# Optimization experiments

Hardware: AMD Instinct MI355X
Metric: run time of the kernel (lower is better)

Reference implementation:

```python
import jax, jax.numpy as jnp
import numpy as np

N, C, Wd, Hd = 16, 64, 128, 128


def setup_inputs() -> dict:
    key = jax.random.key(0)
    k = jax.random.split(key, 6)
    return {
        "xR": jax.random.normal(k[0], (N, C, Wd, Hd), dtype=jnp.float32),
        "xT": jax.random.normal(k[1], (N, C, Wd, Hd), dtype=jnp.float32),
        "WR": jax.random.normal(k[2], (C, C), dtype=jnp.float32) * 0.05,
        "bR": jax.random.normal(k[3], (C,), dtype=jnp.float32) * 0.05,
        "WT": jax.random.normal(k[4], (C, C), dtype=jnp.float32) * 0.05,
        "bT": jax.random.normal(k[5], (C,), dtype=jnp.float32) * 0.05,
    }


def reference(xR, xT, WR, bR, WT, bT):
    n, c, w, h = xR.shape
    wh = w * h
    # 1x1 convs (weight [out_c, in_c]) + bias
    xRa = jnp.einsum('nchw,dc->ndhw', xR, WR) + bR[None, :, None, None]
    xTa = jnp.einsum('nchw,dc->ndhw', xT, WT) + bT[None, :, None, None]
    # [N, WH, C] views of adjusted features
    r = xRa.transpose(0, 2, 3, 1).reshape(n, wh, c)
    t = xTa.transpose(0, 2, 3, 1).reshape(n, wh, c)
    # channel self-attention: [N, C, C] = r^T @ r (reduce over WH)
    rs = jnp.einsum('npc,npd->ncd', r, r)
    ts = jnp.einsum('npc,npd->ncd', t, t)
    # concat along channel-row axis and softmax over the 2C rows
    att = jax.nn.softmax(jnp.concatenate([rs, ts], axis=1), axis=1)  # [N, 2C, C]
    # original (unadjusted) features concatenated along channels: [N, WH, 2C]
    rO = xR.transpose(0, 2, 3, 1).reshape(n, wh, c)
    tO = xT.transpose(0, 2, 3, 1).reshape(n, wh, c)
    xO = jnp.concatenate([rO, tO], axis=2)
    out = jnp.einsum('npk,nkc->npc', xO, att)  # [N, WH, C]
    return out.reshape(n, w, h, c).transpose(0, 3, 1, 2)
```

## Files before the change

### kernel.cpp

```cpp
#include <hip/hip_runtime.h>
#include <math.h>

#define WH 16384

typedef __attribute__((ext_vector_type(8))) short short8;
typedef __attribute__((ext_vector_type(4))) float f32x4;

__device__ __forceinline__ void atomAddF(float* p, float v) {
    __hip_atomic_fetch_add(p, v, __ATOMIC_RELAXED, __HIP_MEMORY_SCOPE_AGENT);
}
__device__ __forceinline__ unsigned short f2bf(float x) {
    unsigned u = __float_as_uint(x);
    u += 0x7fff + ((u >> 16) & 1);
    return (unsigned short)(u >> 16);
}
__device__ __forceinline__ float bf2f(unsigned short h) {
    return __uint_as_float(((unsigned)h) << 16);
}

__global__ void zero_ws_kernel(float* __restrict__ p, int n) {
    int i = blockIdx.x * 256 + threadIdx.x;
    if (i < n) p[i] = 0.f;
}

__global__ __launch_bounds__(256, 2) void gram_kernel(
    const float* __restrict__ xR, const float* __restrict__ xT,
    float* __restrict__ G, float* __restrict__ sv) {
    __shared__ unsigned short shi[16384];
    __shared__ unsigned short slo[16384];
    const int t = threadIdx.x, w = t >> 6, lane = t & 63;
    const int n = blockIdx.y, inp = blockIdx.z;
    const float* __restrict__ X = (inp ? xT : xR) + (size_t)n * 64 * WH;
    float* __restrict__ Gout = G + (size_t)(inp * 16 + n) * 4096;
    float* __restrict__ Sout = sv + (size_t)(inp * 16 + n) * 64;
    const int pbase = blockIdx.x << 10;

    f32x4 acc0 = {0.f, 0.f, 0.f, 0.f}, acc1 = acc0, acc2 = acc0, acc3 = acc0;
    float srow[16];
#pragma unroll
    for (int i = 0; i < 16; ++i) srow[i] = 0.f;

    const int g2 = lane >> 1, halfo = (lane & 1) << 2;
    const int m15 = lane & 15, q = lane >> 4;
    const int cha = (w << 4) + m15;
    const int ch0 = m15, ch1 = 16 + m15, ch2 = 32 + m15, ch3 = 48 + m15;

    float4 vbuf[16];
#pragma unroll
    for (int i = 0; i < 16; ++i) {
        const int r = (i << 2) + w;
        vbuf[i] = *(const float4*)(X + (size_t)r * WH + pbase + (lane << 2));
    }

    for (int tile = 0; tile < 4; ++tile) {
        __syncthreads();
#pragma unroll
        for (int i = 0; i < 16; ++i) {
            const int r = (i << 2) + w;
            const float4 v = vbuf[i];
            srow[i] += v.x + v.y + v.z + v.w;
            const unsigned short h0 = f2bf(v.x), h1 = f2bf(v.y), h2 = f2bf(v.z), h3 = f2bf(v.w);
            const unsigned short l0 = f2bf(v.x - bf2f(h0)), l1 = f2bf(v.y - bf2f(h1)),
                                 l2 = f2bf(v.z - bf2f(h2)), l3 = f2bf(v.w - bf2f(h3));
            const int a = (r << 8) + ((g2 ^ (r & 31)) << 3) + halfo;
            *(ushort4*)&shi[a] = make_ushort4(h0, h1, h2, h3);
            *(ushort4*)&slo[a] = make_ushort4(l0, l1, l2, l3);
        }
        __syncthreads();
        if (tile < 3) {
            const int p1 = pbase + ((tile + 1) << 8);
#pragma unroll
            for (int i = 0; i < 16; ++i) {
                const int r = (i << 2) + w;
                vbuf[i] = *(const float4*)(X + (size_t)r * WH + p1 + (lane << 2));
            }
        }
#pragma unroll
        for (int kk = 0; kk < 8; ++kk) {
            const int grp = (kk << 2) + q;
            const int offa = (cha << 8) + ((grp ^ (cha & 31)) << 3);
            const int off0 = (ch0 << 8) + ((grp ^ (ch0 & 31)) << 3);
            const int off1 = (ch1 << 8) + ((grp ^ (ch1 & 31)) << 3);
            const int off2 = (ch2 << 8) + ((grp ^ (ch2 & 31)) << 3);
            const int off3 = (ch3 << 8) + ((grp ^ (ch3 & 31)) << 3);
            const short8 ah = *(const short8*)&shi[offa];
            const short8 al = *(const short8*)&slo[offa];
            const short8 bh0 = *(const short8*)&shi[off0], bl0 = *(const short8*)&slo[off0];
            const short8 bh1 = *(const short8*)&shi[off1], bl1 = *(const short8*)&slo[off1];
            const short8 bh2 = *(const short8*)&shi[off2], bl2 = *(const short8*)&slo[off2];
            const short8 bh3 = *(const short8*)&shi[off3], bl3 = *(const short8*)&slo[off3];
            acc0 = __builtin_amdgcn_mfma_f32_16x16x32_bf16(ah, bh0, acc0, 0, 0, 0);
            acc0 = __builtin_amdgcn_mfma_f32_16x16x32_bf16(ah, bl0, acc0, 0, 0, 0);
            acc0 = __builtin_amdgcn_mfma_f32_16x16x32_bf16(al, bh0, acc0, 0, 0, 0);
            acc0 = __builtin_amdgcn_mfma_f32_16x16x32_bf16(al, bl0, acc0, 0, 0, 0);
            acc1 = __builtin_amdgcn_mfma_f32_16x16x32_bf16(ah, bh1, acc1, 0, 0, 0);
            acc1 = __builtin_amdgcn_mfma_f32_16x16x32_bf16(ah, bl1, acc1, 0, 0, 0);
            acc1 = __builtin_amdgcn_mfma_f32_16x16x32_bf16(al, bh1, acc1, 0, 0, 0);
            acc1 = __builtin_amdgcn_mfma_f32_16x16x32_bf16(al, bl1, acc1, 0, 0, 0);
            acc2 = __builtin_amdgcn_mfma_f32_16x16x32_bf16(ah, bh2, acc2, 0, 0, 0);
            acc2 = __builtin_amdgcn_mfma_f32_16x16x32_bf16(ah, bl2, acc2, 0, 0, 0);
            acc2 = __builtin_amdgcn_mfma_f32_16x16x32_bf16(al, bh2, acc2, 0, 0, 0);
            acc2 = __builtin_amdgcn_mfma_f32_16x16x32_bf16(al, bl2, acc2, 0, 0, 0);
            acc3 = __builtin_amdgcn_mfma_f32_16x16x32_bf16(ah, bh3, acc3, 0, 0, 0);
            acc3 = __builtin_amdgcn_mfma_f32_16x16x32_bf16(ah, bl3, acc3, 0, 0, 0);
            acc3 = __builtin_amdgcn_mfma_f32_16x16x32_bf16(al, bh3, acc3, 0, 0, 0);
            acc3 = __builtin_amdgcn_mfma_f32_16x16x32_bf16(al, bl3, acc3, 0, 0, 0);
        }
    }
    const int rb = (w << 4) + (q << 2);
#pragma unroll
    for (int r = 0; r < 4; ++r) {
        atomAddF(&Gout[(rb + r) * 64 + 0 + m15], acc0[r]);
        atomAddF(&Gout[(rb + r) * 64 + 16 + m15], acc1[r]);
        atomAddF(&Gout[(rb + r) * 64 + 32 + m15], acc2[r]);
        atomAddF(&Gout[(rb + r) * 64 + 48 + m15], acc3[r]);
    }
#pragma unroll
    for (int i = 0; i < 16; ++i) {
        float v = srow[i];
        for (int m = 32; m >= 1; m >>= 1) v += __shfl_xor(v, m, 64);
        if (lane == 0) atomAddF(&Sout[(i << 2) + w], v);
    }
}

__global__ __launch_bounds__(256) void logits_softmax_kernel(
    const float* __restrict__ WR, const float* __restrict__ bR,
    const float* __restrict__ WT, const float* __restrict__ bT,
    const float* __restrict__ G, const float* __restrict__ sv,
    unsigned short* __restrict__ attb) {
    __shared__ float ldsW[4096];
    __shared__ float ldsWt[4096];
    __shared__ float ldsG[4096];
    __shared__ float ldsL[8192];
    __shared__ float ldsS[64], ldsU[64], ldsMx[64], ldsInv[64];
    const int t = threadIdx.x, n = blockIdx.x;
    for (int inp = 0; inp < 2; ++inp) {
        const float* __restrict__ W = inp ? WT : WR;
        const float* __restrict__ b = inp ? bT : bR;
        const float* __restrict__ Gn = G + (size_t)(inp * 16 + n) * 4096;
        const float* __restrict__ sn = sv + (size_t)(inp * 16 + n) * 64;
        __syncthreads();
#pragma unroll
        for (int m = 0; m < 16; ++m) {
            const int idx = t + (m << 8);
            const float wv = W[idx];
            ldsW[idx] = wv;
            ldsWt[((idx & 63) << 6) + (idx >> 6)] = wv;
            ldsG[idx] = Gn[idx];
        }
        if (t < 64) ldsS[t] = sn[t];
        __syncthreads();
        if (t < 64) {
            float u = 0.f;
            for (int c = 0; c < 64; ++c) u += ldsW[(t << 6) + c] * ldsS[c];
            ldsU[t] = u;
        }
        const int d = t >> 2, e0 = (t & 3) << 4;
        float a[16];
#pragma unroll
        for (int e = 0; e < 16; ++e) a[e] = 0.f;
        for (int c = 0; c < 64; ++c) {
            const float wv = ldsW[(d << 6) + c];
#pragma unroll
            for (int e = 0; e < 16; ++e) a[e] += wv * ldsG[(c << 6) + e0 + e];
        }
        __syncthreads();
#pragma unroll
        for (int e = 0; e < 16; ++e) ldsG[(d << 6) + e0 + e] = a[e];
        __syncthreads();
        float r[16];
#pragma unroll
        for (int e = 0; e < 16; ++e) r[e] = 0.f;
        for (int c = 0; c < 64; ++c) {
            const float m1 = ldsG[(d << 6) + c];
#pragma unroll
            for (int e = 0; e < 16; ++e) r[e] += m1 * ldsWt[(c << 6) + e0 + e];
        }
        const float ud = ldsU[d], bd = b[d];
#pragma unroll
        for (int e = 0; e < 16; ++e) {
            const int ee = e0 + e;
            ldsL[((inp << 6) + d) * 64 + ee] =
                r[e] + ud * b[ee] + bd * ldsU[ee] + 16384.f * bd * b[ee];
        }
    }
    __syncthreads();
    if (t < 64) {
        float mx = -1e30f;
        for (int k = 0; k < 128; ++k) mx = fmaxf(mx, ldsL[(k << 6) + t]);
        float s = 0.f;
        for (int k = 0; k < 128; ++k) s += __expf(ldsL[(k << 6) + t] - mx);
        ldsMx[t] = mx;
        ldsInv[t] = 1.f / s;
    }
    __syncthreads();
    unsigned short* __restrict__ an = attb + (size_t)n * 8192;
#pragma unroll
    for (int i = 0; i < 32; ++i) {
        const int idx = (i << 8) + t;
        const int c = idx & 63;
        an[idx] = f2bf(__expf(ldsL[idx] - ldsMx[c]) * ldsInv[c]);
    }
}

#define FMA4(acc, s, v)        \
    acc.x += (s) * (v).x;      \
    acc.y += (s) * (v).y;      \
    acc.z += (s) * (v).z;      \
    acc.w += (s) * (v).w
__global__ __launch_bounds__(256, 2) void outv_kernel(
    const float* __restrict__ xR, const float* __restrict__ xT,
    const unsigned short* __restrict__ attb, float* __restrict__ out) {
    __shared__ unsigned short lx[32768];
    __shared__ unsigned short la[8192];
    const int t = threadIdx.x, w = t >> 6, lane = t & 63;
    const int n = blockIdx.y;
    const int p0 = blockIdx.x << 8;
    const float* __restrict__ XR = xR + (size_t)n * 64 * WH;
    const float* __restrict__ XT = xT + (size_t)n * 64 * WH;
    const unsigned short* __restrict__ an = attb + (size_t)n * 8192;

    float4 va[16], vb[16];
    ushort4 ab[8];
#pragma unroll
    for (int i = 0; i < 16; ++i) {
        const int k = (i << 2) + w;
        va[i] = *(const float4*)(XR + (size_t)k * WH + p0 + (lane << 2));
    }
#pragma unroll
    for (int i = 0; i < 16; ++i) {
        const int k = (i << 2) + w;
        vb[i] = *(const float4*)(XT + (size_t)k * WH + p0 + (lane << 2));
    }
#pragma unroll
    for (int i = 0; i < 8; ++i) ab[i] = *(const ushort4*)&an[(i << 10) + (t << 2)];
#pragma unroll
    for (int i = 0; i < 16; ++i) {
        const int k = (i << 2) + w;
        const float4 v = va[i];
        *(ushort4*)&lx[(k << 8) + (lane << 2)] =
            make_ushort4(f2bf(v.x), f2bf(v.y), f2bf(v.z), f2bf(v.w));
    }
#pragma unroll
    for (int i = 0; i < 16; ++i) {
        const int k = (i << 2) + w + 64;
        const float4 v = vb[i];
        *(ushort4*)&lx[(k << 8) + (lane << 2)] =
            make_ushort4(f2bf(v.x), f2bf(v.y), f2bf(v.z), f2bf(v.w));
    }
#pragma unroll
    for (int i = 0; i < 8; ++i) {
        const int idx = (i << 10) + (t << 2);
        *(ushort4*)&la[idx] = ab[i];
    }
    __syncthreads();

    const int ci = t >> 5;
    const int pj = t & 31;
    const float4 z4 = make_float4(0.f, 0.f, 0.f, 0.f);
    float4 c00 = z4, c01 = z4, c02 = z4, c03 = z4, c04 = z4, c05 = z4, c06 = z4, c07 = z4;
    float4 c10 = z4, c11 = z4, c12 = z4, c13 = z4, c14 = z4, c15 = z4, c16 = z4, c17 = z4;
#pragma unroll 4
    for (int k = 0; k < 128; ++k) {
        const ushort4 aA = *(const ushort4*)&la[(k << 6) + (ci << 3)];
        const ushort4 aB = *(const ushort4*)&la[(k << 6) + (ci << 3) + 4];
        const ushort4 x0 = *(const ushort4*)&lx[(k << 8) + (pj << 2)];
        const ushort4 x1 = *(const ushort4*)&lx[(k << 8) + 128 + (pj << 2)];
        const float4 v0 = make_float4(bf2f(x0.x), bf2f(x0.y), bf2f(x0.z), bf2f(x0.w));
        const float4 v1 = make_float4(bf2f(x1.x), bf2f(x1.y), bf2f(x1.z), bf2f(x1.w));
        const float a0 = bf2f(aA.x), a1 = bf2f(aA.y), a2 = bf2f(aA.z), a3 = bf2f(aA.w);
        const float a4 = bf2f(aB.x), a5 = bf2f(aB.y), a6 = bf2f(aB.z), a7 = bf2f(aB.w);
        FMA4(c00, a0, v0); FMA4(c10, a0, v1);
        FMA4(c01, a1, v0); FMA4(c11, a1, v1);
        FMA4(c02, a2, v0); FMA4(c12, a2, v1);
        FMA4(c03, a3, v0); FMA4(c13, a3, v1);
        FMA4(c04, a4, v0); FMA4(c14, a4, v1);
        FMA4(c05, a5, v0); FMA4(c15, a5, v1);
        FMA4(c06, a6, v0); FMA4(c16, a6, v1);
        FMA4(c07, a7, v0); FMA4(c17, a7, v1);
    }
    float* __restrict__ on = out + (size_t)n * 64 * WH + p0;
    const int cb = ci << 3;
    const int po = pj << 2;
    *(float4*)(on + (size_t)(cb + 0) * WH + po) = c00;
    *(float4*)(on + (size_t)(cb + 1) * WH + po) = c01;
    *(float4*)(on + (size_t)(cb + 2) * WH + po) = c02;
    *(float4*)(on + (size_t)(cb + 3) * WH + po) = c03;
    *(float4*)(on + (size_t)(cb + 4) * WH + po) = c04;
    *(float4*)(on + (size_t)(cb + 5) * WH + po) = c05;
    *(float4*)(on + (size_t)(cb + 6) * WH + po) = c06;
    *(float4*)(on + (size_t)(cb + 7) * WH + po) = c07;
    *(float4*)(on + (size_t)(cb + 0) * WH + 128 + po) = c10;
    *(float4*)(on + (size_t)(cb + 1) * WH + 128 + po) = c11;
    *(float4*)(on + (size_t)(cb + 2) * WH + 128 + po) = c12;
    *(float4*)(on + (size_t)(cb + 3) * WH + 128 + po) = c13;
    *(float4*)(on + (size_t)(cb + 4) * WH + 128 + po) = c14;
    *(float4*)(on + (size_t)(cb + 5) * WH + 128 + po) = c15;
    *(float4*)(on + (size_t)(cb + 6) * WH + 128 + po) = c16;
    *(float4*)(on + (size_t)(cb + 7) * WH + 128 + po) = c17;
}

extern "C" void kernel_launch(void* const* d_in, const int* in_sizes, int n_in,
                              void* d_out, int out_size, void* d_ws, size_t ws_size,
                              hipStream_t stream) {
    const float* xR = (const float*)d_in[0];
    const float* xT = (const float*)d_in[1];
    const float* WR = (const float*)d_in[2];
    const float* bR = (const float*)d_in[3];
    const float* WT = (const float*)d_in[4];
    const float* bT = (const float*)d_in[5];
    float* out = (float*)d_out;

    float* ws = (float*)d_ws;
    float* G = ws;
    float* sv = ws + 131072;
    unsigned short* attb = (unsigned short*)(ws + 133120);

    zero_ws_kernel<<<520, 256, 0, stream>>>(ws, 133120);
    gram_kernel<<<dim3(16, 16, 2), 256, 0, stream>>>(xR, xT, G, sv);
    logits_softmax_kernel<<<16, 256, 0, stream>>>(WR, bR, WT, bT, G, sv, attb);
    outv_kernel<<<dim3(64, 16), 256, 0, stream>>>(xR, xT, attb, out);
}
```

Before: 276.8 us.

## Use bf16 MFMA for output attention GEMM with swizzled transposed LDS tiles

Replaces the scalar FMA inner loop of the output kernel with 16x16x32 bf16 MFMA instructions. The attention matrix is now written transposed (channel-major) by the softmax kernel, and the input features are staged into LDS transposed (pixel-major) with XOR swizzling to avoid bank conflicts. Global loads of inputs become scalar per-thread column loads instead of float4, and output stores become scalar strided writes, which may reduce memory coalescing efficiency in exchange for much cheaper compute.

```diff
diff --git a/kernel.cpp b/kernel.cpp
--- a/kernel.cpp
+++ b/kernel.cpp
@@ -198,106 +198,106 @@
 #pragma unroll
     for (int i = 0; i < 32; ++i) {
         const int idx = (i << 8) + t;
-        const int c = idx & 63;
-        an[idx] = f2bf(__expf(ldsL[idx] - ldsMx[c]) * ldsInv[c]);
-    }
-}
-
-#define FMA4(acc, s, v)        \
-    acc.x += (s) * (v).x;      \
-    acc.y += (s) * (v).y;      \
-    acc.z += (s) * (v).z;      \
-    acc.w += (s) * (v).w
+        const int k = idx >> 6, c = idx & 63;
+        an[(c << 7) + k] = f2bf(__expf(ldsL[idx] - ldsMx[c]) * ldsInv[c]);
+    }
+}
+
 __global__ __launch_bounds__(256, 2) void outv_kernel(
     const float* __restrict__ xR, const float* __restrict__ xT,
     const unsigned short* __restrict__ attb, float* __restrict__ out) {
-    __shared__ unsigned short lx[32768];
-    __shared__ unsigned short la[8192];
+    __shared__ unsigned short lxT[32768];
+    __shared__ unsigned short lsa[8192];
     const int t = threadIdx.x, w = t >> 6, lane = t & 63;
+    const int m15 = lane & 15, q = lane >> 4;
     const int n = blockIdx.y;
     const int p0 = blockIdx.x << 8;
-    const float* __restrict__ XR = xR + (size_t)n * 64 * WH;
-    const float* __restrict__ XT = xT + (size_t)n * 64 * WH;
+    const float* __restrict__ XR = xR + (size_t)n * 64 * WH + p0 + t;
+    const float* __restrict__ XT = xT + (size_t)n * 64 * WH + p0 + t;
     const unsigned short* __restrict__ an = attb + (size_t)n * 8192;
 
-    float4 va[16], vb[16];
-    ushort4 ab[8];
-#pragma unroll
-    for (int i = 0; i < 16; ++i) {
-        const int k = (i << 2) + w;
-        va[i] = *(const float4*)(XR + (size_t)k * WH + p0 + (lane << 2));
-    }
-#pragma unroll
-    for (int i = 0; i < 16; ++i) {
-        const int k = (i << 2) + w;
-        vb[i] = *(const float4*)(XT + (size_t)k * WH + p0 + (lane << 2));
-    }
-#pragma unroll
-    for (int i = 0; i < 8; ++i) ab[i] = *(const ushort4*)&an[(i << 10) + (t << 2)];
-#pragma unroll
-    for (int i = 0; i < 16; ++i) {
-        const int k = (i << 2) + w;
-        const float4 v = va[i];
-        *(ushort4*)&lx[(k << 8) + (lane << 2)] =
-            make_ushort4(f2bf(v.x), f2bf(v.y), f2bf(v.z), f2bf(v.w));
-    }
-#pragma unroll
-    for (int i = 0; i < 16; ++i) {
-        const int k = (i << 2) + w + 64;
-        const float4 v = vb[i];
-        *(ushort4*)&lx[(k << 8) + (lane << 2)] =
-            make_ushort4(f2bf(v.x), f2bf(v.y), f2bf(v.z), f2bf(v.w));
-    }
 #pragma unroll
     for (int i = 0; i < 8; ++i) {
         const int idx = (i << 10) + (t << 2);
-        *(ushort4*)&la[idx] = ab[i];
+        const ushort4 av = *(const ushort4*)&an[idx];
+        const int c = idx >> 7, ke0 = idx & 127;
+        const int slot = ke0 >> 3;
+        const int wb = (c << 7) + ((slot ^ (c & 15)) << 3) + (ke0 & 7);
+        *(ushort4*)&lsa[wb] = av;
+    }
+    const int pxm = t & 15;
+#pragma unroll
+    for (int c4 = 0; c4 < 4; ++c4) {
+        const float* __restrict__ base = (c4 < 2) ? XR : XT;
+        float v[32];
+#pragma unroll
+        for (int j = 0; j < 32; ++j)
+            v[j] = base[(size_t)((c4 & 1) * 32 + j) * WH];
+#pragma unroll
+        for (int s = 0; s < 4; ++s) {
+            short8 pkt;
+#pragma unroll
+            for (int e = 0; e < 8; ++e) pkt[e] = (short)f2bf(v[(s << 3) + e]);
+            const int slot = (c4 << 2) + s;
+            *(short8*)&lxT[(t << 7) + ((slot ^ pxm) << 3)] = pkt;
+        }
     }
     __syncthreads();
 
-    const int ci = t >> 5;
-    const int pj = t & 31;
-    const float4 z4 = make_float4(0.f, 0.f, 0.f, 0.f);
-    float4 c00 = z4, c01 = z4, c02 = z4, c03 = z4, c04 = z4, c05 = z4, c06 = z4, c07 = z4;
-    float4 c10 = z4, c11 = z4, c12 = z4, c13 = z4, c14 = z4, c15 = z4, c16 = z4, c17 = z4;
-#pragma unroll 4
-    for (int k = 0; k < 128; ++k) {
-        const ushort4 aA = *(const ushort4*)&la[(k << 6) + (ci << 3)];
-        const ushort4 aB = *(const ushort4*)&la[(k << 6) + (ci << 3) + 4];
-        const ushort4 x0 = *(const ushort4*)&lx[(k << 8) + (pj << 2)];
-        const ushort4 x1 = *(const ushort4*)&lx[(k << 8) + 128 + (pj << 2)];
-        const float4 v0 = make_float4(bf2f(x0.x), bf2f(x0.y), bf2f(x0.z), bf2f(x0.w));
-        const float4 v1 = make_float4(bf2f(x1.x), bf2f(x1.y), bf2f(x1.z), bf2f(x1.w));
-        const float a0 = bf2f(aA.x), a1 = bf2f(aA.y), a2 = bf2f(aA.z), a3 = bf2f(aA.w);
-        const float a4 = bf2f(aB.x), a5 = bf2f(aB.y), a6 = bf2f(aB.z), a7 = bf2f(aB.w);
-        FMA4(c00, a0, v0); FMA4(c10, a0, v1);
-        FMA4(c01, a1, v0); FMA4(c11, a1, v1);
-        FMA4(c02, a2, v0); FMA4(c12, a2, v1);
-        FMA4(c03, a3, v0); FMA4(c13, a3, v1);
-        FMA4(c04, a4, v0); FMA4(c14, a4, v1);
-        FMA4(c05, a5, v0); FMA4(c15, a5, v1);
-        FMA4(c06, a6, v0); FMA4(c16, a6, v1);
-        FMA4(c07, a7, v0); FMA4(c17, a7, v1);
+    f32x4 z = {0.f, 0.f, 0.f, 0.f};
+    f32x4 a00 = z, a01 = z, a02 = z, a03 = z;
+    f32x4 a10 = z, a11 = z, a12 = z, a13 = z;
+    f32x4 a20 = z, a21 = z, a22 = z, a23 = z;
+    f32x4 a30 = z, a31 = z, a32 = z, a33 = z;
+    const int rA0 = (0 * 16 + m15) << 7, rA1 = (1 * 16 + m15) << 7;
+    const int rA2 = (2 * 16 + m15) << 7, rA3 = (3 * 16 + m15) << 7;
+    const int rB0 = (((w << 2) + 0) * 16 + m15) << 7;
+    const int rB1 = (((w << 2) + 1) * 16 + m15) << 7;
+    const int rB2 = (((w << 2) + 2) * 16 + m15) << 7;
+    const int rB3 = (((w << 2) + 3) * 16 + m15) << 7;
+#pragma unroll
+    for (int kg = 0; kg < 4; ++kg) {
+        const int sx = (((kg << 2) + q) ^ m15) << 3;
+        const short8 A0 = *(const short8*)&lsa[rA0 + sx];
+        const short8 A1 = *(const short8*)&lsa[rA1 + sx];
+        const short8 A2 = *(const short8*)&lsa[rA2 + sx];
+        const short8 A3 = *(const short8*)&lsa[rA3 + sx];
+        const short8 B0 = *(const short8*)&lxT[rB0 + sx];
+        const short8 B1 = *(const short8*)&lxT[rB1 + sx];
+        const short8 B2 = *(const short8*)&lxT[rB2 + sx];
+        const short8 B3 = *(const short8*)&lxT[rB3 + sx];
+        a00 = __builtin_amdgcn_mfma_f32_16x16x32_bf16(A0, B0, a00, 0, 0, 0);
+        a01 = __builtin_amdgcn_mfma_f32_16x16x32_bf16(A0, B1, a01, 0, 0, 0);
+        a02 = __builtin_amdgcn_mfma_f32_16x16x32_bf16(A0, B2, a02, 0, 0, 0);
+        a03 = __builtin_amdgcn_mfma_f32_16x16x32_bf16(A0, B3, a03, 0, 0, 0);
+        a10 = __builtin_amdgcn_mfma_f32_16x16x32_bf16(A1, B0, a10, 0, 0, 0);
+        a11 = __builtin_amdgcn_mfma_f32_16x16x32_bf16(A1, B1, a11, 0, 0, 0);
+        a12 = __builtin_amdgcn_mfma_f32_16x16x32_bf16(A1, B2, a12, 0, 0, 0);
+        a13 = __builtin_amdgcn_mfma_f32_16x16x32_bf16(A1, B3, a13, 0, 0, 0);
+        a20 = __builtin_amdgcn_mfma_f32_16x16x32_bf16(A2, B0, a20, 0, 0, 0);
+        a21 = __builtin_amdgcn_mfma_f32_16x16x32_bf16(A2, B1, a21, 0, 0, 0);
+        a22 = __builtin_amdgcn_mfma_f32_16x16x32_bf16(A2, B2, a22, 0, 0, 0);
+        a23 = __builtin_amdgcn_mfma_f32_16x16x32_bf16(A2, B3, a23, 0, 0, 0);
+        a30 = __builtin_amdgcn_mfma_f32_16x16x32_bf16(A3, B0, a30, 0, 0, 0);
+        a31 = __builtin_amdgcn_mfma_f32_16x16x32_bf16(A3, B1, a31, 0, 0, 0);
+        a32 = __builtin_amdgcn_mfma_f32_16x16x32_bf16(A3, B2, a32, 0, 0, 0);
+        a33 = __builtin_amdgcn_mfma_f32_16x16x32_bf16(A3, B3, a33, 0, 0, 0);
     }
     float* __restrict__ on = out + (size_t)n * 64 * WH + p0;
-    const int cb = ci << 3;
-    const int po = pj << 2;
-    *(float4*)(on + (size_t)(cb + 0) * WH + po) = c00;
-    *(float4*)(on + (size_t)(cb + 1) * WH + po) = c01;
-    *(float4*)(on + (size_t)(cb + 2) * WH + po) = c02;
-    *(float4*)(on + (size_t)(cb + 3) * WH + po) = c03;
-    *(float4*)(on + (size_t)(cb + 4) * WH + po) = c04;
-    *(float4*)(on + (size_t)(cb + 5) * WH + po) = c05;
-    *(float4*)(on + (size_t)(cb + 6) * WH + po) = c06;
-    *(float4*)(on + (size_t)(cb + 7) * WH + po) = c07;
-    *(float4*)(on + (size_t)(cb + 0) * WH + 128 + po) = c10;
-    *(float4*)(on + (size_t)(cb + 1) * WH + 128 + po) = c11;
-    *(float4*)(on + (size_t)(cb + 2) * WH + 128 + po) = c12;
-    *(float4*)(on + (size_t)(cb + 3) * WH + 128 + po) = c13;
-    *(float4*)(on + (size_t)(cb + 4) * WH + 128 + po) = c14;
-    *(float4*)(on + (size_t)(cb + 5) * WH + 128 + po) = c15;
-    *(float4*)(on + (size_t)(cb + 6) * WH + 128 + po) = c16;
-    *(float4*)(on + (size_t)(cb + 7) * WH + 128 + po) = c17;
+#define ST(accv, mt, j)                                                          \
+    {                                                                            \
+        float* bp = on + (size_t)(((mt) << 4) + (q << 2)) * WH +                 \
+                    (((w << 2) + (j)) << 4) + m15;                               \
+        bp[0] = accv[0];                                                         \
+        bp[WH] = accv[1];                                                        \
+        bp[2 * WH] = accv[2];                                                    \
+        bp[3 * WH] = accv[3];                                                    \
+    }
+    ST(a00, 0, 0); ST(a01, 0, 1); ST(a02, 0, 2); ST(a03, 0, 3);
+    ST(a10, 1, 0); ST(a11, 1, 1); ST(a12, 1, 2); ST(a13, 1, 3);
+    ST(a20, 2, 0); ST(a21, 2, 1); ST(a22, 2, 2); ST(a23, 2, 3);
+    ST(a30, 3, 0); ST(a31, 3, 1); ST(a32, 3, 2); ST(a33, 3, 3);
+#undef ST
 }
 
 extern "C" void kernel_launch(void* const* d_in, const int* in_sizes, int n_in,
```

Result: faster. 246.3 us (-11.0%).
